# Optimization experiments

Hardware: AMD Instinct MI355X
Metric: run time of the kernel (lower is better)

## Reference

```python
import jax, jax.numpy as jnp
import numpy as np

N, D_IN, D_HID, D_OUT, E, STEPS = 50000, 64, 64, 32, 800000, 3


def setup_inputs() -> dict:
    key = jax.random.key(0)
    ks = jax.random.split(key, 8)
    x = jax.random.normal(ks[0], (N, D_IN), dtype=jnp.float32)
    edge_index = jax.random.randint(ks[1], (2, E), 0, N, dtype=jnp.int32)
    s1 = 1.0 / np.sqrt(2 * D_IN)
    s2 = 1.0 / np.sqrt(D_IN)
    s3 = 1.0 / np.sqrt(2 * D_HID)
    s4 = 1.0 / np.sqrt(D_HID)
    W_att1 = jax.random.uniform(ks[2], (2 * D_IN, 1), jnp.float32, -s1, s1)
    b_att1 = jax.random.uniform(ks[3], (1,), jnp.float32, -s1, s1)
    W_lin1 = jax.random.uniform(ks[4], (D_IN, D_HID), jnp.float32, -s2, s2)
    W_att2 = jax.random.uniform(ks[5], (2 * D_HID, 1), jnp.float32, -s3, s3)
    b_att2 = jax.random.uniform(ks[6], (1,), jnp.float32, -s3, s3)
    W_lin2 = jax.random.uniform(ks[7], (D_HID, D_OUT), jnp.float32, -s4, s4)
    return {"x": x, "edge_index": edge_index, "W_att1": W_att1, "b_att1": b_att1,
            "W_lin1": W_lin1, "W_att2": W_att2, "b_att2": b_att2, "W_lin2": W_lin2}


def _aggregate_mean(h, src, dst, n):
    # mean over incoming neighbors; nodes with no in-edges get 0 (clamped denom)
    feat_sum = jax.ops.segment_sum(h[src], dst, num_segments=n)
    deg = jax.ops.segment_sum(jnp.ones_like(src, dtype=h.dtype), dst, num_segments=n)
    return feat_sum / jnp.maximum(deg, 1.0)[:, None]


def _gcn_conv(x, src, dst, W_att, b_att, W_lin, n):
    h_src = x[src]                       # [E, d]
    h_dst = x[dst]                       # [E, d]
    score = jax.nn.leaky_relu(
        jnp.concatenate([h_src, h_dst], axis=-1) @ W_att + b_att)  # [E, 1]
    weighted = score * (h_src @ W_lin)   # [E, d_out]
    feats = jax.ops.segment_sum(weighted, dst, num_segments=n)
    att = jax.ops.segment_sum(jnp.abs(weighted), dst, num_segments=n)
    return feats, att


def reference(x, edge_index, W_att1, b_att1, W_lin1, W_att2, b_att2, W_lin2):
    src, dst = edge_index[0], edge_index[1]
    n = x.shape[0]
    # graphSmoothing positional encoding: stack of [x, mean^1(x), ..., mean^S(x)], then mean over steps
    h = x
    acc = x
    for _ in range(STEPS):
        h = _aggregate_mean(h, src, dst, n)
        acc = acc + h
    xs = acc / (STEPS + 1)
    h1, _att1 = _gcn_conv(xs, src, dst, W_att1, b_att1, W_lin1, n)
    h1 = jax.nn.relu(h1)  # dropout is identity in eval mode
    out, _att2 = _gcn_conv(h1, src, dst, W_att2, b_att2, W_lin2, n)
    # y=None -> loss_separation = loss_focus = 0
    return out
```

## Files before the change

### kernel.cpp

```cpp
#include <hip/hip_runtime.h>


typedef __attribute__((ext_vector_type(8))) _Float16 half8;

#define CHUNK 2048

__global__ void binA_kernel(const int* __restrict__ src, const int* __restrict__ dst,
                            unsigned int* __restrict__ packed, int* __restrict__ offs,
                            const float* __restrict__ x, _Float16* __restrict__ x16,
                            int total8, int E) {
    __shared__ int cnt[256];
    __shared__ int pref[256];
    __shared__ int cur[256];
    __shared__ unsigned int stage[CHUNK];
    int t = threadIdx.x;
    int base = blockIdx.x * CHUNK;
    int len = E - base; if (len > CHUNK) len = CHUNK;
    cnt[t] = 0;
    __syncthreads();
    for (int i = t; i < len; i += 256) atomicAdd(&cnt[dst[base + i] >> 8], 1);
    __syncthreads();
    int v = cnt[t];
    pref[t] = v;
    __syncthreads();
    for (int off = 1; off < 256; off <<= 1) {
        int u = (t >= off) ? pref[t - off] : 0;
        __syncthreads();
        pref[t] += u;
        __syncthreads();
    }
    int excl = pref[t] - v;
    cur[t] = excl;
    offs[blockIdx.x * 257 + t] = excl;
    if (t == 255) offs[blockIdx.x * 257 + 256] = pref[255];
    __syncthreads();
    for (int i = t; i < len; i += 256) {
        int s = src[base + i], d = dst[base + i];
        int pos = atomicAdd(&cur[d >> 8], 1);
        stage[pos] = (unsigned int)s | ((unsigned int)d << 16);
    }
    __syncthreads();
    for (int i = t; i < len; i += 256) packed[base + i] = stage[i];
    for (int i = blockIdx.x * 256 + t; i < total8; i += gridDim.x * 256) {
        float4 v0 = ((const float4*)x)[2 * i];
        float4 v1 = ((const float4*)x)[2 * i + 1];
        half8 o;
        o[0] = (_Float16)v0.x; o[1] = (_Float16)v0.y; o[2] = (_Float16)v0.z; o[3] = (_Float16)v0.w;
        o[4] = (_Float16)v1.x; o[5] = (_Float16)v1.y; o[6] = (_Float16)v1.z; o[7] = (_Float16)v1.w;
        ((half8*)x16)[i] = o;
    }
}

__global__ void binB_count_kernel(const unsigned int* __restrict__ packed,
                                  const int* __restrict__ offs,
                                  int* __restrict__ deg, int* __restrict__ partTot,
                                  int nChunks, int N) {
    __shared__ int cnt[256];
    __shared__ int red[256];
    int t = threadIdx.x;
    int p = blockIdx.x;
    cnt[t] = 0;
    __syncthreads();
    for (int c = t; c < nChunks; c += 256) {
        const int* oc = offs + c * 257;
        int o0 = oc[p], o1 = oc[p + 1];
        const unsigned int* pk = packed + (size_t)c * CHUNK;
        for (int i = o0; i < o1; ++i) atomicAdd(&cnt[(pk[i] >> 16) & 255], 1);
    }
    __syncthreads();
    int node = p * 256 + t;
    int c = cnt[t];
    if (node < N) deg[node] = c;
    red[t] = (c + 3) & ~3;
    __syncthreads();
    for (int off = 128; off > 0; off >>= 1) {
        if (t < off) red[t] += red[t + off];
        __syncthreads();
    }
    if (t == 0) partTot[p] = red[0];
}

__global__ void binB_scatter_kernel(const unsigned int* __restrict__ packed,
                                    const int* __restrict__ offs, const int* __restrict__ deg,
                                    const int* __restrict__ partTot, int* __restrict__ row_ptr,
                                    unsigned short* __restrict__ src_idx, int nChunks,
                                    int nPart, int N) {
    __shared__ int ps[256];
    __shared__ int pref[256];
    __shared__ int cur[256];
    int t = threadIdx.x;
    int p = blockIdx.x;
    ps[t] = (t < nPart) ? partTot[t] : 0;
    __syncthreads();
    for (int off = 1; off < 256; off <<= 1) {
        int u = (t >= off) ? ps[t - off] : 0;
        __syncthreads();
        ps[t] += u;
        __syncthreads();
    }
    int partBase = (p > 0) ? ps[p - 1] : 0;
    int node = p * 256 + t;
    int d = (node < N) ? deg[node] : 0;
    int a = (d + 3) & ~3;
    pref[t] = a;
    __syncthreads();
    for (int off = 1; off < 256; off <<= 1) {
        int u = (t >= off) ? pref[t - off] : 0;
        __syncthreads();
        pref[t] += u;
        __syncthreads();
    }
    int rp = partBase + pref[t] - a;
    if (node < N) row_ptr[node] = rp;
    cur[t] = rp;
    __syncthreads();
    for (int c = t; c < nChunks; c += 256) {
        const int* oc = offs + c * 257;
        int o0 = oc[p], o1 = oc[p + 1];
        const unsigned int* pk = packed + (size_t)c * CHUNK;
        for (int i = o0; i < o1; ++i) {
            unsigned int pr = pk[i];
            int ln = (pr >> 16) & 255;
            int slot = atomicAdd(&cur[ln], 1);
            src_idx[slot] = (unsigned short)(pr & 0xffffu);
        }
    }
}

__global__ void agg_mean8_kernel(const _Float16* __restrict__ h, const int* __restrict__ row_ptr,
                                 const int* __restrict__ degp,
                                 const unsigned short* __restrict__ src_idx,
                                 _Float16* __restrict__ h_out, int N) {
    int wid = (blockIdx.x * blockDim.x + threadIdx.x) >> 6;
    int lane = threadIdx.x & 63;
    int node = wid * 2 + (lane >> 5);
    if (node >= N) return;
    int lane32 = lane & 31;
    int beg = row_ptr[node];
    int dgr = degp[node];
    int end = beg + dgr;
    int j = lane32 >> 3, f = lane32 & 7;
    const uint4* rowp = (const uint4*)h;
    float acc[8];
    #pragma unroll
    for (int q = 0; q < 8; ++q) acc[q] = 0.f;
    for (int base = beg + 4 * j; base < end; base += 16) {
        ushort4 i4 = *(const ushort4*)(src_idx + base);
        unsigned short ss[4] = {i4.x, i4.y, i4.z, i4.w};
        #pragma unroll
        for (int k = 0; k < 4; ++k) {
            int e = base + k;
            int s = ss[k];
            uint4 raw = rowp[(size_t)s * 8 + f];
            if (e >= end) { raw.x = 0u; raw.y = 0u; raw.z = 0u; raw.w = 0u; }
            half8 v = *(half8*)&raw;
            #pragma unroll
            for (int q = 0; q < 8; ++q) acc[q] += (float)v[q];
        }
    }
    #pragma unroll
    for (int q = 0; q < 8; ++q) {
        acc[q] += __shfl_down(acc[q], 16, 64);
        acc[q] += __shfl_down(acc[q], 8, 64);
    }
    if (lane32 < 8) {
        float inv = dgr > 0 ? 1.f / (float)dgr : 0.f;
        half8 o;
        #pragma unroll
        for (int q = 0; q < 8; ++q) o[q] = (_Float16)(acc[q] * inv);
        *((half8*)h_out + (size_t)node * 8 + lane32) = o;
    }
}

__global__ void mean3_xf1_kernel(const _Float16* __restrict__ h ,
                                 const _Float16* __restrict__ x16,
                                 const _Float16* __restrict__ hA ,
                                 const int* __restrict__ row_ptr, const int* __restrict__ degp,
                                 const unsigned short* __restrict__ src_idx,
                                 const float* __restrict__ W_lin1,
                                 const float* __restrict__ W_att1,
                                 _Float16* __restrict__ z1, float* __restrict__ a1,
                                 float* __restrict__ a2, int N) {
    __shared__ float Wl[64 * 64];
    __shared__ float Wa[128];
    for (int i = threadIdx.x; i < 64 * 64; i += 256) Wl[i] = W_lin1[i];
    if (threadIdx.x < 128) Wa[threadIdx.x] = W_att1[threadIdx.x];
    __syncthreads();
    int wid = (blockIdx.x * blockDim.x + threadIdx.x) >> 6;
    int lane = threadIdx.x & 63;
    int node = wid * 2 + (lane >> 5);
    if (node >= N) return;
    int lane32 = lane & 31;
    int beg = row_ptr[node];
    int dgr = degp[node];
    int end = beg + dgr;
    int j = lane32 >> 3, f = lane32 & 7;
    const uint4* rowp = (const uint4*)h;
    float acc[8];
    #pragma unroll
    for (int q = 0; q < 8; ++q) acc[q] = 0.f;
    for (int base = beg + 4 * j; base < end; base += 16) {
        ushort4 i4 = *(const ushort4*)(src_idx + base);
        unsigned short ss[4] = {i4.x, i4.y, i4.z, i4.w};
        #pragma unroll
        for (int k = 0; k < 4; ++k) {
            int e = base + k;
            int s = ss[k];
            uint4 raw = rowp[(size_t)s * 8 + f];
            if (e >= end) { raw.x = 0u; raw.y = 0u; raw.z = 0u; raw.w = 0u; }
            half8 v = *(half8*)&raw;
            #pragma unroll
            for (int q = 0; q < 8; ++q) acc[q] += (float)v[q];
        }
    }
    #pragma unroll
    for (int q = 0; q < 8; ++q) {
        acc[q] += __shfl_down(acc[q], 16, 64);
        acc[q] += __shfl_down(acc[q], 8, 64);
    }
    float xs[8];
    #pragma unroll
    for (int q = 0; q < 8; ++q) xs[q] = 0.f;
    float p1 = 0.f, p2 = 0.f;
    if (lane32 < 8) {
        float inv = dgr > 0 ? 1.f / (float)dgr : 0.f;
        half8 xv = *((const half8*)x16 + (size_t)node * 8 + f);
        half8 h1v = *((const half8*)hA + (size_t)node * 8 + f);
        half8 h2v = *((const half8*)h + (size_t)node * 8 + f);
        #pragma unroll
        for (int q = 0; q < 8; ++q) {
            xs[q] = ((float)xv[q] + (float)h1v[q] + (float)h2v[q] + acc[q] * inv) * 0.25f;
            p1 += xs[q] * Wa[f * 8 + q];
            p2 += xs[q] * Wa[64 + f * 8 + q];
        }
    }
    p1 += __shfl_down(p1, 4, 64); p2 += __shfl_down(p2, 4, 64);
    p1 += __shfl_down(p1, 2, 64); p2 += __shfl_down(p2, 2, 64);
    p1 += __shfl_down(p1, 1, 64); p2 += __shfl_down(p2, 1, 64);
    if (lane32 == 0) { a1[node] = p1; a2[node] = p2; }
    float z0 = 0.f, zb = 0.f;
    int srcBase = lane & 32;
    #pragma unroll
    for (int k = 0; k < 64; ++k) {
        float xk = __shfl(xs[k & 7], srcBase + (k >> 3), 64);
        z0 += xk * Wl[k * 64 + lane32];
        zb += xk * Wl[k * 64 + 32 + lane32];
    }
    z1[(size_t)node * 64 + lane32] = (_Float16)z0;
    z1[(size_t)node * 64 + 32 + lane32] = (_Float16)zb;
}

__global__ void conv64_xf2_kernel(const _Float16* __restrict__ z, const float* __restrict__ a1v,
                                  const float* __restrict__ a2v, const float* __restrict__ b_att,
                                  const int* __restrict__ row_ptr, const int* __restrict__ degp,
                                  const unsigned short* __restrict__ src_idx,
                                  const float* __restrict__ W_lin2,
                                  const float* __restrict__ W_att2,
                                  float* __restrict__ z2, float* __restrict__ a1o,
                                  float* __restrict__ a2o, int N) {
    __shared__ float Wl[64 * 32];
    __shared__ float Wa[128];
    for (int i = threadIdx.x; i < 64 * 32; i += 256) Wl[i] = W_lin2[i];
    if (threadIdx.x < 128) Wa[threadIdx.x] = W_att2[threadIdx.x];
    __syncthreads();
    int wid = (blockIdx.x * blockDim.x + threadIdx.x) >> 6;
    int lane = threadIdx.x & 63;
    int node = wid * 2 + (lane >> 5);
    if (node >= N) return;
    int lane32 = lane & 31;
    float ad = a2v[node] + b_att[0];
    int beg = row_ptr[node];
    int dgr = degp[node];
    int end = beg + dgr;
    int j = lane32 >> 3, f = lane32 & 7;
    const uint4* rowp = (const uint4*)z;
    float acc[8];
    #pragma unroll
    for (int q = 0; q < 8; ++q) acc[q] = 0.f;
    for (int base = beg + 4 * j; base < end; base += 16) {
        ushort4 i4 = *(const ushort4*)(src_idx + base);
        unsigned short ss[4] = {i4.x, i4.y, i4.z, i4.w};
        #pragma unroll
        for (int k = 0; k < 4; ++k) {
            int e = base + k;
            int s = ss[k];
            float sc = a1v[s] + ad;
            sc = sc > 0.f ? sc : 0.01f * sc;
            uint4 raw = rowp[(size_t)s * 8 + f];
            if (e >= end) { raw.x = 0u; raw.y = 0u; raw.z = 0u; raw.w = 0u; }
            half8 v = *(half8*)&raw;
            #pragma unroll
            for (int q = 0; q < 8; ++q) acc[q] += sc * (float)v[q];
        }
    }
    #pragma unroll
    for (int q = 0; q < 8; ++q) {
        acc[q] += __shfl_down(acc[q], 16, 64);
        acc[q] += __shfl_down(acc[q], 8, 64);
    }
    float hreg[8];
    #pragma unroll
    for (int q = 0; q < 8; ++q) hreg[q] = 0.f;
    float p1 = 0.f, p2 = 0.f;
    if (lane32 < 8) {
        #pragma unroll
        for (int q = 0; q < 8; ++q) {
            hreg[q] = fmaxf(acc[q], 0.f);
            p1 += hreg[q] * Wa[f * 8 + q];
            p2 += hreg[q] * Wa[64 + f * 8 + q];
        }
    }
    p1 += __shfl_down(p1, 4, 64); p2 += __shfl_down(p2, 4, 64);
    p1 += __shfl_down(p1, 2, 64); p2 += __shfl_down(p2, 2, 64);
    p1 += __shfl_down(p1, 1, 64); p2 += __shfl_down(p2, 1, 64);
    if (lane32 == 0) { a1o[node] = p1; a2o[node] = p2; }
    float zacc = 0.f;
    int srcBase = lane & 32;
    #pragma unroll
    for (int k = 0; k < 64; ++k) {
        float hk = __shfl(hreg[k & 7], srcBase + (k >> 3), 64);
        zacc += hk * Wl[k * 32 + lane32];
    }
    z2[(size_t)node * 32 + lane32] = zacc;
}

__global__ void agg_conv32_kernel(const float* __restrict__ z, const float* __restrict__ a1v,
                                  const float* __restrict__ a2v, const float* __restrict__ b_att,
                                  const int* __restrict__ row_ptr, const int* __restrict__ degp,
                                  const unsigned short* __restrict__ src_idx,
                                  float* __restrict__ outp, int N) {
    int wid = (blockIdx.x * blockDim.x + threadIdx.x) >> 6;
    int lane = threadIdx.x & 63;
    int node = wid * 2 + (lane >> 5);
    if (node >= N) return;
    int lane32 = lane & 31;
    float ad = a2v[node] + b_att[0];
    int beg = row_ptr[node];
    int end = beg + degp[node];
    int j = lane32 >> 3, f = lane32 & 7;
    const float4* rowp = (const float4*)z;
    float ax = 0.f, ay = 0.f, az = 0.f, aw = 0.f;
    for (int base = beg + 4 * j; base < end; base += 16) {
        ushort4 i4 = *(const ushort4*)(src_idx + base);
        unsigned short ss[4] = {i4.x, i4.y, i4.z, i4.w};
        #pragma unroll
        for (int k = 0; k < 4; ++k) {
            int e = base + k;
            int s = ss[k];
            float sc = a1v[s] + ad;
            sc = sc > 0.f ? sc : 0.01f * sc;
            if (e >= end) sc = 0.f;
            float4 v = rowp[(size_t)s * 8 + f];
            ax += sc * v.x; ay += sc * v.y; az += sc * v.z; aw += sc * v.w;
        }
    }
    ax += __shfl_down(ax, 16, 64); ay += __shfl_down(ay, 16, 64);
    az += __shfl_down(az, 16, 64); aw += __shfl_down(aw, 16, 64);
    ax += __shfl_down(ax, 8, 64);  ay += __shfl_down(ay, 8, 64);
    az += __shfl_down(az, 8, 64);  aw += __shfl_down(aw, 8, 64);
    if (lane32 < 8) {
        float4 o; o.x = ax; o.y = ay; o.z = az; o.w = aw;
        *((float4*)(outp + (size_t)node * 32) + lane32) = o;
    }
}

extern "C" void kernel_launch(void* const* d_in, const int* in_sizes, int n_in,
                              void* d_out, int out_size, void* d_ws, size_t ws_size,
                              hipStream_t stream) {
    const float* x      = (const float*)d_in[0];
    const int*   ei     = (const int*)d_in[1];
    const float* W_att1 = (const float*)d_in[2];
    const float* b_att1 = (const float*)d_in[3];
    const float* W_lin1 = (const float*)d_in[4];
    const float* W_att2 = (const float*)d_in[5];
    const float* b_att2 = (const float*)d_in[6];
    const float* W_lin2 = (const float*)d_in[7];
    float* out = (float*)d_out;

    int N = in_sizes[0] / 64;
    int E = in_sizes[1] / 2;
    const int* src = ei;
    const int* dst = ei + E;
    int nChunks = (E + CHUNK - 1) / CHUNK;
    int nPart   = (N + 255) >> 8;

    char* ws = (char*)d_ws;
    size_t off = 0;
    auto alloc = [&](size_t bytes) -> void* {
        void* p = ws + off;
        off += (bytes + 255) & ~(size_t)255;
        return p;
    };
    int*            deg     = (int*)alloc((size_t)N * 4);
    int*            row_ptr = (int*)alloc((size_t)N * 4);
    unsigned short* src_idx = (unsigned short*)alloc(((size_t)E + 4 * N) * 2);
    unsigned int*   packed  = (unsigned int*)alloc((size_t)nChunks * CHUNK * 4);
    int*            offs    = (int*)alloc((size_t)nChunks * 257 * 4);
    int*            partTot = (int*)alloc((size_t)256 * 4);
    _Float16* x16 = (_Float16*)alloc((size_t)N * 64 * 2);
    _Float16* hA  = (_Float16*)alloc((size_t)N * 64 * 2);
    _Float16* hB  = (_Float16*)alloc((size_t)N * 64 * 2);
    _Float16* z1  = (_Float16*)alloc((size_t)N * 64 * 2);
    float* z2  = (float*)alloc((size_t)N * 32 * 4);
    float* a1  = (float*)alloc((size_t)N * 4);
    float* a2  = (float*)alloc((size_t)N * 4);
    float* a1b = (float*)alloc((size_t)N * 4);
    float* a2b = (float*)alloc((size_t)N * 4);

    const int tb = 256;
    int total8 = N * 8;

    binA_kernel<<<nChunks, 256, 0, stream>>>(src, dst, packed, offs, x, x16, total8, E);
    binB_count_kernel<<<nPart, 256, 0, stream>>>(packed, offs, deg, partTot, nChunks, N);
    binB_scatter_kernel<<<nPart, 256, 0, stream>>>(packed, offs, deg, partTot, row_ptr,
                                                   src_idx, nChunks, nPart, N);

    int gBlocks = (N + 7) / 8;
    agg_mean8_kernel<<<gBlocks, tb, 0, stream>>>(x16, row_ptr, deg, src_idx, hA, N);
    agg_mean8_kernel<<<gBlocks, tb, 0, stream>>>(hA,  row_ptr, deg, src_idx, hB, N);
    mean3_xf1_kernel<<<gBlocks, tb, 0, stream>>>(hB, x16, hA, row_ptr, deg, src_idx,
                                                 W_lin1, W_att1, z1, a1, a2, N);
    conv64_xf2_kernel<<<gBlocks, tb, 0, stream>>>(z1, a1, a2, b_att1, row_ptr, deg, src_idx,
                                                  W_lin2, W_att2, z2, a1b, a2b, N);
    agg_conv32_kernel<<<gBlocks, tb, 0, stream>>>(z2, a1b, a2b, b_att2, row_ptr, deg, src_idx,
                                                  out, N);
}
```

Before: 242.1 us.

## Split fused gather+transform kernels into separate aggregation and dense transform kernels

Unfuses the per-node linear transforms from the gather kernels. Aggregation kernels now write xs and relu(h1) as fp16 buffers, and two new one-wavefront-per-node kernels do the 64x64 and 64x32 matmuls and the attention projections, reading weights directly from global memory instead of staging them in LDS. This removes the per-block 16KB LDS weight load and its barrier from the gather kernels, which should improve their occupancy. In exchange it adds two kernel launches and an extra write and read of two N x 64 fp16 intermediates.

```diff
diff --git a/kernel.cpp b/kernel.cpp
--- a/kernel.cpp
+++ b/kernel.cpp
@@ -172,20 +172,14 @@
     }
 }
 
-__global__ void mean3_xf1_kernel(const _Float16* __restrict__ h ,
-                                 const _Float16* __restrict__ x16,
-                                 const _Float16* __restrict__ hA ,
-                                 const int* __restrict__ row_ptr, const int* __restrict__ degp,
-                                 const unsigned short* __restrict__ src_idx,
-                                 const float* __restrict__ W_lin1,
-                                 const float* __restrict__ W_att1,
-                                 _Float16* __restrict__ z1, float* __restrict__ a1,
-                                 float* __restrict__ a2, int N) {
-    __shared__ float Wl[64 * 64];
-    __shared__ float Wa[128];
-    for (int i = threadIdx.x; i < 64 * 64; i += 256) Wl[i] = W_lin1[i];
-    if (threadIdx.x < 128) Wa[threadIdx.x] = W_att1[threadIdx.x];
-    __syncthreads();
+__global__ void mean3_xs_kernel(const _Float16* __restrict__ h ,
+                                const _Float16* __restrict__ x16,
+                                const _Float16* __restrict__ hA ,
+                                const int* __restrict__ row_ptr, const int* __restrict__ degp,
+                                const unsigned short* __restrict__ src_idx,
+                                const float* __restrict__ W_att1,
+                                _Float16* __restrict__ xs16, float* __restrict__ a1,
+                                float* __restrict__ a2, int N) {
     int wid = (blockIdx.x * blockDim.x + threadIdx.x) >> 6;
     int lane = threadIdx.x & 63;
     int node = wid * 2 + (lane >> 5);
@@ -218,51 +212,49 @@
         acc[q] += __shfl_down(acc[q], 16, 64);
         acc[q] += __shfl_down(acc[q], 8, 64);
     }
-    float xs[8];
-    #pragma unroll
-    for (int q = 0; q < 8; ++q) xs[q] = 0.f;
     float p1 = 0.f, p2 = 0.f;
     if (lane32 < 8) {
         float inv = dgr > 0 ? 1.f / (float)dgr : 0.f;
         half8 xv = *((const half8*)x16 + (size_t)node * 8 + f);
         half8 h1v = *((const half8*)hA + (size_t)node * 8 + f);
         half8 h2v = *((const half8*)h + (size_t)node * 8 + f);
+        half8 o;
         #pragma unroll
         for (int q = 0; q < 8; ++q) {
-            xs[q] = ((float)xv[q] + (float)h1v[q] + (float)h2v[q] + acc[q] * inv) * 0.25f;
-            p1 += xs[q] * Wa[f * 8 + q];
-            p2 += xs[q] * Wa[64 + f * 8 + q];
-        }
+            float xsv = ((float)xv[q] + (float)h1v[q] + (float)h2v[q] + acc[q] * inv) * 0.25f;
+            o[q] = (_Float16)xsv;
+            p1 += xsv * W_att1[f * 8 + q];
+            p2 += xsv * W_att1[64 + f * 8 + q];
+        }
+        *((half8*)xs16 + (size_t)node * 8 + f) = o;
     }
     p1 += __shfl_down(p1, 4, 64); p2 += __shfl_down(p2, 4, 64);
     p1 += __shfl_down(p1, 2, 64); p2 += __shfl_down(p2, 2, 64);
     p1 += __shfl_down(p1, 1, 64); p2 += __shfl_down(p2, 1, 64);
     if (lane32 == 0) { a1[node] = p1; a2[node] = p2; }
-    float z0 = 0.f, zb = 0.f;
-    int srcBase = lane & 32;
+}
+
+__global__ void xform1z_kernel(const _Float16* __restrict__ xs16,
+                               const float* __restrict__ W_lin1,
+                               _Float16* __restrict__ z1, int N) {
+    int n = (blockIdx.x * blockDim.x + threadIdx.x) >> 6;
+    int lane = threadIdx.x & 63;
+    if (n >= N) return;
+    float xv = (float)xs16[(size_t)n * 64 + lane];
+    float acc = 0.f;
     #pragma unroll
     for (int k = 0; k < 64; ++k) {
-        float xk = __shfl(xs[k & 7], srcBase + (k >> 3), 64);
-        z0 += xk * Wl[k * 64 + lane32];
-        zb += xk * Wl[k * 64 + 32 + lane32];
-    }
-    z1[(size_t)node * 64 + lane32] = (_Float16)z0;
-    z1[(size_t)node * 64 + 32 + lane32] = (_Float16)zb;
-}
-
-__global__ void conv64_xf2_kernel(const _Float16* __restrict__ z, const float* __restrict__ a1v,
+        float xk = __shfl(xv, k, 64);
+        acc += xk * W_lin1[k * 64 + lane];
+    }
+    z1[(size_t)n * 64 + lane] = (_Float16)acc;
+}
+
+__global__ void agg_conv64_kernel(const _Float16* __restrict__ z, const float* __restrict__ a1v,
                                   const float* __restrict__ a2v, const float* __restrict__ b_att,
                                   const int* __restrict__ row_ptr, const int* __restrict__ degp,
                                   const unsigned short* __restrict__ src_idx,
-                                  const float* __restrict__ W_lin2,
-                                  const float* __restrict__ W_att2,
-                                  float* __restrict__ z2, float* __restrict__ a1o,
-                                  float* __restrict__ a2o, int N) {
-    __shared__ float Wl[64 * 32];
-    __shared__ float Wa[128];
-    for (int i = threadIdx.x; i < 64 * 32; i += 256) Wl[i] = W_lin2[i];
-    if (threadIdx.x < 128) Wa[threadIdx.x] = W_att2[threadIdx.x];
-    __syncthreads();
+                                  _Float16* __restrict__ h1out, int N) {
     int wid = (blockIdx.x * blockDim.x + threadIdx.x) >> 6;
     int lane = threadIdx.x & 63;
     int node = wid * 2 + (lane >> 5);
@@ -270,8 +262,7 @@
     int lane32 = lane & 31;
     float ad = a2v[node] + b_att[0];
     int beg = row_ptr[node];
-    int dgr = degp[node];
-    int end = beg + dgr;
+    int end = beg + degp[node];
     int j = lane32 >> 3, f = lane32 & 7;
     const uint4* rowp = (const uint4*)z;
     float acc[8];
@@ -298,30 +289,38 @@
         acc[q] += __shfl_down(acc[q], 16, 64);
         acc[q] += __shfl_down(acc[q], 8, 64);
     }
-    float hreg[8];
-    #pragma unroll
-    for (int q = 0; q < 8; ++q) hreg[q] = 0.f;
-    float p1 = 0.f, p2 = 0.f;
     if (lane32 < 8) {
-        #pragma unroll
-        for (int q = 0; q < 8; ++q) {
-            hreg[q] = fmaxf(acc[q], 0.f);
-            p1 += hreg[q] * Wa[f * 8 + q];
-            p2 += hreg[q] * Wa[64 + f * 8 + q];
-        }
-    }
-    p1 += __shfl_down(p1, 4, 64); p2 += __shfl_down(p2, 4, 64);
-    p1 += __shfl_down(p1, 2, 64); p2 += __shfl_down(p2, 2, 64);
-    p1 += __shfl_down(p1, 1, 64); p2 += __shfl_down(p2, 1, 64);
-    if (lane32 == 0) { a1o[node] = p1; a2o[node] = p2; }
-    float zacc = 0.f;
-    int srcBase = lane & 32;
+        half8 o;
+        #pragma unroll
+        for (int q = 0; q < 8; ++q) o[q] = (_Float16)fmaxf(acc[q], 0.f);
+        *((half8*)h1out + (size_t)node * 8 + lane32) = o;
+    }
+}
+
+__global__ void xform2z_kernel(const _Float16* __restrict__ h1,
+                               const float* __restrict__ W_lin2,
+                               const float* __restrict__ W_att2,
+                               float* __restrict__ z2, float* __restrict__ a1o,
+                               float* __restrict__ a2o, int N) {
+    int n = (blockIdx.x * blockDim.x + threadIdx.x) >> 6;
+    int lane = threadIdx.x & 63;
+    if (n >= N) return;
+    float hv = (float)h1[(size_t)n * 64 + lane];
+    float p1 = hv * W_att2[lane];
+    float p2 = hv * W_att2[64 + lane];
+    for (int off = 32; off > 0; off >>= 1) {
+        p1 += __shfl_down(p1, off, 64);
+        p2 += __shfl_down(p2, off, 64);
+    }
+    if (lane == 0) { a1o[n] = p1; a2o[n] = p2; }
+    float acc = 0.f;
+    int lane32 = lane & 31;
     #pragma unroll
     for (int k = 0; k < 64; ++k) {
-        float hk = __shfl(hreg[k & 7], srcBase + (k >> 3), 64);
-        zacc += hk * Wl[k * 32 + lane32];
-    }
-    z2[(size_t)node * 32 + lane32] = zacc;
+        float hk = __shfl(hv, k, 64);
+        if (lane < 32) acc += hk * W_lin2[k * 32 + lane32];
+    }
+    if (lane < 32) z2[(size_t)n * 32 + lane32] = acc;
 }
 
 __global__ void agg_conv32_kernel(const float* __restrict__ z, const float* __restrict__ a1v,
@@ -400,7 +399,9 @@
     _Float16* x16 = (_Float16*)alloc((size_t)N * 64 * 2);
     _Float16* hA  = (_Float16*)alloc((size_t)N * 64 * 2);
     _Float16* hB  = (_Float16*)alloc((size_t)N * 64 * 2);
+    _Float16* xs16 = (_Float16*)alloc((size_t)N * 64 * 2);
     _Float16* z1  = (_Float16*)alloc((size_t)N * 64 * 2);
+    _Float16* h1f = (_Float16*)alloc((size_t)N * 64 * 2);
     float* z2  = (float*)alloc((size_t)N * 32 * 4);
     float* a1  = (float*)alloc((size_t)N * 4);
     float* a2  = (float*)alloc((size_t)N * 4);
@@ -416,12 +417,15 @@
                                                    src_idx, nChunks, nPart, N);
 
     int gBlocks = (N + 7) / 8;
+    int xBlocks = (N + 3) / 4;
     agg_mean8_kernel<<<gBlocks, tb, 0, stream>>>(x16, row_ptr, deg, src_idx, hA, N);
     agg_mean8_kernel<<<gBlocks, tb, 0, stream>>>(hA,  row_ptr, deg, src_idx, hB, N);
-    mean3_xf1_kernel<<<gBlocks, tb, 0, stream>>>(hB, x16, hA, row_ptr, deg, src_idx,
-                                                 W_lin1, W_att1, z1, a1, a2, N);
-    conv64_xf2_kernel<<<gBlocks, tb, 0, stream>>>(z1, a1, a2, b_att1, row_ptr, deg, src_idx,
-                                                  W_lin2, W_att2, z2, a1b, a2b, N);
+    mean3_xs_kernel<<<gBlocks, tb, 0, stream>>>(hB, x16, hA, row_ptr, deg, src_idx,
+                                                W_att1, xs16, a1, a2, N);
+    xform1z_kernel<<<xBlocks, tb, 0, stream>>>(xs16, W_lin1, z1, N);
+    agg_conv64_kernel<<<gBlocks, tb, 0, stream>>>(z1, a1, a2, b_att1, row_ptr, deg, src_idx,
+                                                  h1f, N);
+    xform2z_kernel<<<xBlocks, tb, 0, stream>>>(h1f, W_lin2, W_att2, z2, a1b, a2b, N);
     agg_conv32_kernel<<<gBlocks, tb, 0, stream>>>(z2, a1b, a2b, b_att2, row_ptr, deg, src_idx,
                                                   out, N);
 }
```

After: 294.0 us. 21.4% more time.
